# Kernel tuning notes

Measured on AMD Instinct MI355X. Metric: run time of the kernel, lower is better.

## Reference

```python
import jax, jax.numpy as jnp
import numpy as np
from jax import lax

B, C, H, W = 4, 256, 64, 64
O = 256
EPS = 1e-5


def setup_inputs() -> dict:
    key = jax.random.key(0)
    ks = jax.random.split(key, 20)
    s = 0.02
    d = {
        'input1': jax.random.normal(ks[0], (B, C, H, W), jnp.float32),
        'input2': jax.random.normal(ks[1], (B, C, H, W), jnp.float32),
        'wq1': jax.random.normal(ks[2], (C // 8, C), jnp.float32) * s,
        'bq1': jnp.zeros((C // 8,), jnp.float32),
        'wk1': jax.random.normal(ks[3], (C // 4, C), jnp.float32) * s,
        'bk1': jnp.zeros((C // 4,), jnp.float32),
        'wv1': jax.random.normal(ks[4], (C, C), jnp.float32) * s,
        'bv1': jnp.zeros((C,), jnp.float32),
        'wq2': jax.random.normal(ks[5], (C // 8, C), jnp.float32) * s,
        'bq2': jnp.zeros((C // 8,), jnp.float32),
        'wk2': jax.random.normal(ks[6], (C // 4, C), jnp.float32) * s,
        'bk2': jnp.zeros((C // 4,), jnp.float32),
        'wv2': jax.random.normal(ks[7], (C, C), jnp.float32) * s,
        'bv2': jnp.zeros((C,), jnp.float32),
        'gamma': jnp.asarray([0.1], jnp.float32),
        'w_cat': jax.random.normal(ks[8], (O, 2 * C, 3, 3), jnp.float32) * s,
        'bn_scale': jnp.ones((O,), jnp.float32),
        'bn_bias': jnp.zeros((O,), jnp.float32),
        'bn_mean': jnp.zeros((O,), jnp.float32),
        'bn_var': jnp.ones((O,), jnp.float32),
    }
    return d


def _conv1x1(x, w, b):
    # x: [B,C,H,W], w: [Co,C] -> [B,Co,H,W]
    return jnp.einsum('bchw,oc->bohw', x, w) + b[None, :, None, None]


def reference(input1, input2, wq1, bq1, wk1, bk1, wv1, bv1,
              wq2, bq2, wk2, bk2, wv2, bv2, gamma, w_cat,
              bn_scale, bn_bias, bn_mean, bn_var):
    b, c, h, w = input1.shape
    hw = h * w
    q1 = _conv1x1(input1, wq1, bq1)
    k1 = _conv1x1(input1, wk1, bk1).reshape(b, -1, hw)
    v1 = _conv1x1(input1, wv1, bv1).reshape(b, -1, hw)
    q2 = _conv1x1(input2, wq2, bq2)
    k2 = _conv1x1(input2, wk2, bk2).reshape(b, -1, hw)
    v2 = _conv1x1(input2, wv2, bv2).reshape(b, -1, hw)
    # concat q heads along channel -> [B, C/4, HW] -> [B, HW, C/4]
    q = jnp.concatenate([q1, q2], axis=1).reshape(b, -1, hw).transpose(0, 2, 1)
    # branch 1: [B,HW,HW] scores (no scaling, as in source)
    attn1 = jax.nn.softmax(jnp.einsum('bnc,bcm->bnm', q, k1), axis=-1)
    out1 = jnp.einsum('bcm,bnm->bcn', v1, attn1).reshape(b, c, h, w)
    out1 = gamma[0] * out1 + input1
    # branch 2
    attn2 = jax.nn.softmax(jnp.einsum('bnc,bcm->bnm', q, k2), axis=-1)
    out2 = jnp.einsum('bcm,bnm->bcn', v2, attn2).reshape(b, c, h, w)
    out2 = gamma[0] * out2 + input2
    # conv_cat: 3x3 conv (no bias) + BatchNorm (eval stats) + ReLU
    cat = jnp.concatenate([out1, out2], axis=1)
    conv = lax.conv_general_dilated(cat, w_cat, (1, 1), 'SAME',
                                    dimension_numbers=('NCHW', 'OIHW', 'NCHW'))
    inv = bn_scale / jnp.sqrt(bn_var + EPS)
    bn = conv * inv[None, :, None, None] + (bn_bias - bn_mean * inv)[None, :, None, None]
    feat_sum = jax.nn.relu(bn)
    return (feat_sum, out1, out2)
```

## Files before the change

### kernel.cpp

```cpp
#include <hip/hip_runtime.h>
#include <hip/hip_bf16.h>

#define HW 4096

#define KT_OFF   1048576
#define WTP_OFF  1572864
#define O1_OFF   4194304
#define WVB_OFF  1179648
#define XBF_OFF  1310720
#define WS_NEED  19398656ull
#define WS_NEED2 20463616ull

typedef short v8s  __attribute__((ext_vector_type(8)));
typedef float v16f __attribute__((ext_vector_type(16)));

#define LSTR 72
#define ZSTR 264
#define CPAD 20
#define PL_ROWS 128
#define PL_SZ  (2 * PL_ROWS * LSTR)
#define XP_SZ  (2 * 256 * LSTR)
#define XLHALF (4 * 66 * CPAD)
#define CPYCH  69696
#define CPYB   2230272
#define V5SL   4224

__device__ __forceinline__ unsigned short f2b(float f) {
    unsigned u = __float_as_uint(f);
    return (unsigned short)((u + 0x7fffu + ((u >> 16) & 1u)) >> 16);
}
__device__ __forceinline__ unsigned cvt_pk_bf16(float lo, float hi) {
    float2 f2; f2.x = lo; f2.y = hi;
    __hip_bfloat162 h = __float22bfloat162_rn(f2);
    unsigned r;
    __builtin_memcpy(&r, &h, 4);
    return r;
}
__device__ __forceinline__ v8s load8(const unsigned short* p) {
    union { uint2 u[2]; v8s v; } t;
    t.u[0] = *(const uint2*)p;
    t.u[1] = *(const uint2*)(p + 4);
    return t.v;
}

__global__ __launch_bounds__(256) void wprep_proj(
    const float* __restrict__ wq1, const float* __restrict__ wk1, const float* __restrict__ wv1,
    const float* __restrict__ wq2, const float* __restrict__ wk2, const float* __restrict__ wv2,
    float* __restrict__ wtp) {
    int idx = blockIdx.x * 256 + threadIdx.x;
    if (idx >= 2 * 256 * 352) return;
    int sel = idx / 90112;
    int r   = idx - sel * 90112;
    int c   = r / 352;
    int co  = r - c * 352;
    const float* w; int row;
    if (co < 32)      { w = sel ? wq2 : wq1; row = co; }
    else if (co < 96) { w = sel ? wk2 : wk1; row = co - 32; }
    else              { w = sel ? wv2 : wv1; row = co - 96; }
    wtp[idx] = w[row * 256 + c];
}

__global__ __launch_bounds__(256) void wprep_convw(const float* __restrict__ wcat,
                                                   unsigned short* __restrict__ wt) {
    int i = blockIdx.x * 256 + threadIdx.x;
    if (i >= 32 * 9 * 256 * 16) return;
    const int ci_l = i & 15;
    const int o    = (i >> 4) & 255;
    const int t2   = i >> 12;
    const int tap  = t2 % 9;
    const int chunk = t2 / 9;
    wt[i] = f2b(wcat[((size_t)o * 512 + chunk * 16 + ci_l) * 9 + tap]);
}

__global__ __launch_bounds__(256) void wprep_wv(const float* __restrict__ wv1,
                                                const float* __restrict__ wv2,
                                                unsigned short* __restrict__ out) {
    int i = blockIdx.x * 256 + threadIdx.x;
    if (i >= 131072) return;
    const float* src = (i < 65536) ? wv1 : wv2;
    out[i] = f2b(src[i & 65535]);
}

__global__ __launch_bounds__(256) void wprep_xbf(const float* __restrict__ x1,
                                                 const float* __restrict__ x2,
                                                 unsigned short* __restrict__ xbf) {
    const size_t e = ((size_t)blockIdx.x * 256 + threadIdx.x) * 8;
    if (e >= 8388608) return;
    const float* src = (e < 4194304) ? (x1 + e) : (x2 + (e - 4194304));
    const float4 a = *(const float4*)src;
    const float4 c = *(const float4*)(src + 4);
    uint4 o;
    o.x = cvt_pk_bf16(a.x, a.y); o.y = cvt_pk_bf16(a.z, a.w);
    o.z = cvt_pk_bf16(c.x, c.y); o.w = cvt_pk_bf16(c.z, c.w);
    *(uint4*)&xbf[e] = o;
}

__global__ __launch_bounds__(256) void proj_kernel(
    const float* __restrict__ x1, const float* __restrict__ x2,
    const float* __restrict__ bq1, const float* __restrict__ bk1,
    const float* __restrict__ bq2, const float* __restrict__ bk2,
    float* __restrict__ dout) {
    __shared__ __align__(16) float xls[256][64];
    const int tile = blockIdx.x, sel = blockIdx.y, b = blockIdx.z;
    const int n0 = tile * 64;
    const float* xb = (sel ? x2 : x1) + (size_t)b * 256 * HW;

    for (int i = threadIdx.x; i < 4096; i += 256) {
        const int row = i >> 4, c4 = (i & 15) * 4;
        *(float4*)&xls[row][c4] = *(const float4*)(xb + (size_t)row * HW + n0 + c4);
    }
    __syncthreads();

    const int n   = threadIdx.x & 63;
    const int cog = __builtin_amdgcn_readfirstlane(threadIdx.x >> 6);
    const float* bq = sel ? bq2 : bq1;
    const float* bk = sel ? bk2 : bk1;
    const float* wc = dout + WTP_OFF + (size_t)sel * 90112;
    unsigned short* qtg = (unsigned short*)dout + (size_t)b * HW * 64;
    unsigned short* ktg = (unsigned short*)dout + KT_OFF + (size_t)(sel * 4 + b) * HW * 64;

    for (int blk = 0; blk < 3; ++blk) {
        const int co0 = cog * 24 + blk * 8;
        float acc[8];
        const float* brow; int r0; bool isq;
        if (co0 < 32) { r0 = co0;      brow = bq; isq = true;  }
        else          { r0 = co0 - 32; brow = bk; isq = false; }
        #pragma unroll
        for (int k = 0; k < 8; ++k) acc[k] = brow[r0 + k];
        #pragma unroll 4
        for (int c = 0; c < 256; ++c) {
            const float xv = xls[c][n];
            const float4 w0 = *(const float4*)(wc + (size_t)c * 352 + co0);
            const float4 w1 = *(const float4*)(wc + (size_t)c * 352 + co0 + 4);
            acc[0] += xv * w0.x; acc[1] += xv * w0.y; acc[2] += xv * w0.z; acc[3] += xv * w0.w;
            acc[4] += xv * w1.x; acc[5] += xv * w1.y; acc[6] += xv * w1.z; acc[7] += xv * w1.w;
        }
        unsigned pk2[4];
        #pragma unroll
        for (int k = 0; k < 4; ++k) pk2[k] = cvt_pk_bf16(acc[2 * k], acc[2 * k + 1]);
        unsigned short* dst = isq ? (qtg + (size_t)(n0 + n) * 64 + sel * 32 + r0)
                                  : (ktg + (size_t)(n0 + n) * 64 + r0);
        *(uint4*)dst = *(const uint4*)pk2;
    }
}

template <int USEBF>
__global__ __launch_bounds__(512, 2) void attn_kernel(
    const float* __restrict__ in1, const float* __restrict__ in2,
    const unsigned short* __restrict__ xbf,
    const unsigned short* __restrict__ wvbf,
    const float* __restrict__ bv1, const float* __restrict__ bv2,
    const float* __restrict__ gamma_p,
    float* __restrict__ dout) {
    __shared__ __align__(16) unsigned short smem[PL_SZ + XP_SZ];
    __shared__ float rsums[128][2];
    __shared__ float lfin[128];

    const int bid = blockIdx.x;
    const int g   = bid & 7;
    const int qt  = bid >> 3;
    const int br  = g >> 2, b = g & 3;
    const int t = threadIdx.x;
    const int w = t >> 6, lane = t & 63, h = lane >> 5, l32 = lane & 31;

    const unsigned short* qtg = (const unsigned short*)dout + (size_t)b * HW * 64;
    const unsigned short* ktg = (const unsigned short*)dout + KT_OFF + (size_t)(br * 4 + b) * HW * 64;
    const float* xg = (br ? in2 : in1) + (size_t)b * 256 * HW;
    float* zo = dout + O1_OFF + (size_t)br * 4194304 + (size_t)b * 256 * HW;

    const int msub = (w & 1) * 32;
    const int nsub = (w >> 1) * 32;
    const int cs   = w & 3;
    const int nh   = w >> 2;
    const int koff = h * 8;

    unsigned short* plds = smem;
    unsigned short* xp   = smem + PL_SZ;

    v8s aq[4];
    #pragma unroll
    for (int ks = 0; ks < 4; ++ks)
        aq[ks] = *(const v8s*)(qtg + (size_t)(qt * 128 + nsub + l32) * 64 + ks * 16 + koff);

    const unsigned short* kpt = ktg + (size_t)(msub + l32) * 64 + koff;
    v8s kf[4];
    #pragma unroll
    for (int ks = 0; ks < 4; ++ks)
        kf[ks] = *(const v8s*)(kpt + ks * 16);

    const int m4 = (t & 15) * 4, r0i = t >> 4;
    const float* xgp = xg + (size_t)r0i * HW + m4;
    const unsigned short* xbp = xbf + (size_t)br * 4194304
                              + (size_t)b * 256 * HW + (size_t)r0i * HW + m4;

    uint2 xpk[8];
    if constexpr (USEBF) {
        #pragma unroll
        for (int j = 0; j < 8; ++j) xpk[j] = *(const uint2*)(xbp + (size_t)j * 32 * HW);
    } else {
        float4 xr0[8];
        #pragma unroll
        for (int j = 0; j < 8; ++j) xr0[j] = *(const float4*)(xgp + (size_t)j * 32 * HW);
        #pragma unroll
        for (int j = 0; j < 8; ++j) {
            xpk[j].x = cvt_pk_bf16(xr0[j].x, xr0[j].y);
            xpk[j].y = cvt_pk_bf16(xr0[j].z, xr0[j].w);
        }
    }

    v16f a00, a01, a10, a11;
    #pragma unroll
    for (int i = 0; i < 16; ++i) { a00[i] = 0.f; a01[i] = 0.f; a10[i] = 0.f; a11[i] = 0.f; }
    float racc = 0.f;

    #pragma unroll 1
    for (int mt = 0; mt < 64; ++mt) {
        const int cur = mt & 1;
        v16f s;
        #pragma unroll
        for (int i = 0; i < 16; ++i) s[i] = 0.f;
        #pragma unroll
        for (int ks = 0; ks < 4; ++ks)
            s = __builtin_amdgcn_mfma_f32_32x32x16_bf16(kf[ks], aq[ks], s, 0, 0, 0);
        const int mg = (mt < 63) ? (mt + 1) * 64 : 0;
        #pragma unroll
        for (int ks = 0; ks < 4; ++ks)
            kf[ks] = *(const v8s*)(kpt + (size_t)mg * 64 + ks * 16);
        float4 xr[8];
        if constexpr (!USEBF) {
            #pragma unroll
            for (int j = 0; j < 8; ++j)
                xr[j] = *(const float4*)(xgp + (size_t)j * 32 * HW + mg);
        }
        unsigned short* prow = plds + (size_t)(cur * PL_ROWS + nsub + l32) * LSTR + msub;
        #pragma unroll
        for (int rp = 0; rp < 8; ++rp) {
            const float e0 = __expf(s[2 * rp]);
            const float e1 = __expf(s[2 * rp + 1]);
            racc += e0 + e1;
            const int m0 = ((2 * rp) & 3) + 8 * (rp >> 1) + 4 * h;
            *(unsigned*)&prow[m0] = cvt_pk_bf16(e0, e1);
        }
        {
            unsigned short* xw = xp + (size_t)(cur * 256 + r0i) * LSTR + m4;
            #pragma unroll
            for (int j = 0; j < 8; ++j)
                *(uint2*)(xw + (size_t)j * 32 * LSTR) = xpk[j];
        }
        if constexpr (USEBF) {
            #pragma unroll
            for (int j = 0; j < 8; ++j)
                xpk[j] = *(const uint2*)(xbp + (size_t)j * 32 * HW + mg);
        }
        __syncthreads();
        {
            const unsigned short* xb0 = xp + (size_t)(cur * 256 + cs * 64 + l32) * LSTR;
            const unsigned short* xb1 = xb0 + (size_t)32 * LSTR;
            const unsigned short* pb0 = plds + (size_t)(cur * PL_ROWS + nh * 64 + l32) * LSTR;
            const unsigned short* pb1 = pb0 + (size_t)32 * LSTR;
            #pragma unroll
            for (int ks = 0; ks < 4; ++ks) {
                const int mo = ks * 16 + koff;
                const v8s xa0 = *(const v8s*)(xb0 + mo);
                const v8s xa1 = *(const v8s*)(xb1 + mo);
                const v8s pf0 = *(const v8s*)(pb0 + mo);
                const v8s pf1 = *(const v8s*)(pb1 + mo);
                a00 = __builtin_amdgcn_mfma_f32_32x32x16_bf16(xa0, pf0, a00, 0, 0, 0);
                a01 = __builtin_amdgcn_mfma_f32_32x32x16_bf16(xa0, pf1, a01, 0, 0, 0);
                a10 = __builtin_amdgcn_mfma_f32_32x32x16_bf16(xa1, pf0, a10, 0, 0, 0);
                a11 = __builtin_amdgcn_mfma_f32_32x32x16_bf16(xa1, pf1, a11, 0, 0, 0);
            }
        }
        if constexpr (!USEBF) {
            #pragma unroll
            for (int j = 0; j < 8; ++j) {
                xpk[j].x = cvt_pk_bf16(xr[j].x, xr[j].y);
                xpk[j].y = cvt_pk_bf16(xr[j].z, xr[j].w);
            }
        }
    }
    __syncthreads();
    {
        const float rtot = racc + __shfl_xor(racc, 32);
        if (lane < 32) rsums[nsub + l32][w & 1] = rtot;
    }
    __syncthreads();
    if (t < 128) lfin[t] = 1.0f / (rsums[t][0] + rsums[t][1]);
    __syncthreads();
    const float dn0 = lfin[nh * 64 + l32];
    const float dn1 = lfin[nh * 64 + 32 + l32];
    unsigned short (*zt)[ZSTR] = (unsigned short (*)[ZSTR])smem;
    #pragma unroll
    for (int rp = 0; rp < 8; ++rp) {
        const int r = rp * 2;
        const int c = cs * 64 + (r & 3) + 8 * (r >> 2) + 4 * h;
        const int n0r = nh * 64 + l32, n1r = nh * 64 + 32 + l32;
        *(unsigned*)&zt[n0r][c]      = cvt_pk_bf16(a00[r] * dn0, a00[r + 1] * dn0);
        *(unsigned*)&zt[n1r][c]      = cvt_pk_bf16(a01[r] * dn1, a01[r + 1] * dn1);
        *(unsigned*)&zt[n0r][c + 32] = cvt_pk_bf16(a10[r] * dn0, a10[r + 1] * dn0);
        *(unsigned*)&zt[n1r][c + 32] = cvt_pk_bf16(a11[r] * dn1, a11[r + 1] * dn1);
    }
    __syncthreads();
    const unsigned short* wvb = wvbf + (size_t)br * 65536;
    const float* bvp = br ? bv2 : bv1;
    const float gamma = gamma_p[0];
    const int ob = cs * 64;
    const int ncol = qt * 128 + nh * 64;
    v16f m00, m01, m10, m11;
    #pragma unroll
    for (int i = 0; i < 16; ++i) { m00[i] = 0.f; m01[i] = 0.f; m10[i] = 0.f; m11[i] = 0.f; }
    #pragma unroll
    for (int ks = 0; ks < 16; ++ks) {
        const int k = ks * 16 + koff;
        const v8s aA = *(const v8s*)(wvb + (size_t)(ob + l32) * 256 + k);
        const v8s aB = *(const v8s*)(wvb + (size_t)(ob + 32 + l32) * 256 + k);
        const v8s b0v = *(const v8s*)&zt[nh * 64 + l32][k];
        const v8s b1v = *(const v8s*)&zt[nh * 64 + 32 + l32][k];
        m00 = __builtin_amdgcn_mfma_f32_32x32x16_bf16(aA, b0v, m00, 0, 0, 0);
        m01 = __builtin_amdgcn_mfma_f32_32x32x16_bf16(aA, b1v, m01, 0, 0, 0);
        m10 = __builtin_amdgcn_mfma_f32_32x32x16_bf16(aB, b0v, m10, 0, 0, 0);
        m11 = __builtin_amdgcn_mfma_f32_32x32x16_bf16(aB, b1v, m11, 0, 0, 0);
    }
    #pragma unroll
    for (int r = 0; r < 16; ++r) {
        const int o = ob + (r & 3) + 8 * (r >> 2) + 4 * h;
        const float bvA = bvp[o], bvB = bvp[o + 32];
        const size_t base0 = (size_t)o * HW + ncol;
        const size_t base1 = (size_t)(o + 32) * HW + ncol;
        zo[base0 + l32]      = gamma * (m00[r] + bvA) + xg[base0 + l32];
        zo[base0 + 32 + l32] = gamma * (m01[r] + bvA) + xg[base0 + 32 + l32];
        zo[base1 + l32]      = gamma * (m10[r] + bvB) + xg[base1 + l32];
        zo[base1 + 32 + l32] = gamma * (m11[r] + bvB) + xg[base1 + 32 + l32];
    }
}

__global__ __launch_bounds__(256) void cpy_pad(const float* __restrict__ dsrc,
                                               unsigned short* __restrict__ cpy) {
    __shared__ float xls[16][65];
    const int hp = blockIdx.x, chunk = blockIdx.y, b = blockIdx.z;
    const int t = threadIdx.x;
    unsigned short* crow = cpy + (((size_t)(b * 32 + chunk) * 66 + hp) * 66) * 16;
    if (hp == 0 || hp == 65) {
        if (t < 132) *(uint4*)(crow + t * 8) = make_uint4(0, 0, 0, 0);
        return;
    }
    const int hh = hp - 1;
    const float* src = dsrc + O1_OFF + (size_t)(chunk < 16 ? 0 : 1) * 4194304
                     + (size_t)b * 1048576 + (size_t)((chunk & 15) * 16) * HW + (size_t)hh * 64;
    {
        const int ci = t >> 6, ww = t & 63;
        #pragma unroll
        for (int j = 0; j < 4; ++j)
            xls[ci + 4 * j][ww] = src[(size_t)(ci + 4 * j) * HW + ww];
    }
    __syncthreads();
    {
        const int wwp = t >> 2, q = t & 3;
        uint2 pk;
        pk.x = cvt_pk_bf16(xls[q * 4 + 0][wwp], xls[q * 4 + 1][wwp]);
        pk.y = cvt_pk_bf16(xls[q * 4 + 2][wwp], xls[q * 4 + 3][wwp]);
        *(uint2*)(crow + (size_t)(wwp + 1) * 16 + q * 4) = pk;
    }
    if (t < 4) {
        unsigned short* p = crow + (size_t)(t >> 1) * 65 * 16 + (t & 1) * 8;
        *(uint4*)p = make_uint4(0, 0, 0, 0);
    }
}

__global__ __launch_bounds__(256, 4) void conv_v5(
    const unsigned short* __restrict__ wt,
    const unsigned short* __restrict__ cpy,
    const float* __restrict__ bn_scale, const float* __restrict__ bn_bias,
    const float* __restrict__ bn_mean,  const float* __restrict__ bn_var,
    float* __restrict__ dout) {
    __shared__ __align__(16) unsigned short xl[2][V5SL];

    const int bid = blockIdx.x;
    const int lin = (bid & 7) * 128 + (bid >> 3);
    const int ot  = lin & 7;
    const int g   = lin >> 3;
    const int pt  = g & 31, b = g >> 5;
    const int h0  = pt * 2;
    const int t   = threadIdx.x;
    const int w   = t >> 6, lane = t & 63, h = lane >> 5, l32 = lane & 31;
    const int px  = w * 32 + l32;
    const int r0  = px >> 6, c0 = px & 63;

    const unsigned short* cb = cpy + (size_t)b * CPYB + (size_t)h0 * 66 * 16;
    const unsigned short* wb = wt + (size_t)(ot * 32 + l32) * 16 + h * 8;

    v16f acc;
    #pragma unroll
    for (int i = 0; i < 16; ++i) acc[i] = 0.f;

    uint4 xs[3]; bool xv[3];
    #pragma unroll
    for (int j = 0; j < 3; ++j) {
        const int idx = j * 256 + t;
        xv[j] = idx < 528;
        if (xv[j]) xs[j] = *(const uint4*)(cb + (size_t)idx * 8);
    }

    #pragma unroll 1
    for (int chunk = 0; chunk < 32; ++chunk) {
        const int cur = chunk & 1;
        #pragma unroll
        for (int j = 0; j < 3; ++j)
            if (xv[j]) *(uint4*)&xl[cur][(size_t)(j * 256 + t) * 8] = xs[j];
        v8s wf[9];
        {
            const unsigned short* wc = wb + (size_t)chunk * 36864;
            #pragma unroll
            for (int tap = 0; tap < 9; ++tap)
                wf[tap] = *(const v8s*)(wc + (size_t)tap * 4096);
        }
        if (chunk < 31) {
            const unsigned short* cn = cb + (size_t)(chunk + 1) * CPYCH;
            #pragma unroll
            for (int j = 0; j < 3; ++j)
                if (xv[j]) xs[j] = *(const uint4*)(cn + (size_t)(j * 256 + t) * 8);
        }
        __syncthreads();
        #pragma unroll
        for (int dy = 0; dy < 3; ++dy) {
            #pragma unroll
            for (int dx = 0; dx < 3; ++dx) {
                const v8s bf = *(const v8s*)&xl[cur][(size_t)((r0 + dy) * 66 + c0 + dx) * 16 + h * 8];
                acc = __builtin_amdgcn_mfma_f32_32x32x16_bf16(wf[dy * 3 + dx], bf, acc, 0, 0, 0);
            }
        }
    }
    const size_t gp = (size_t)(h0 + r0) * 64 + c0;
    #pragma unroll
    for (int r = 0; r < 16; ++r) {
        const int o_g = ot * 32 + (r & 3) + 8 * (r >> 2) + 4 * h;
        const float iv = bn_scale[o_g] * __frsqrt_rn(bn_var[o_g] + 1e-5f);
        const float ad = bn_bias[o_g] - bn_mean[o_g] * iv;
        float v = acc[r] * iv + ad;
        v = v > 0.f ? v : 0.f;
        dout[((size_t)b * 256 + o_g) * HW + gp] = v;
    }
}

__global__ __launch_bounds__(256) void conv_kernel(
    const unsigned short* __restrict__ wt,
    const float* __restrict__ bn_scale, const float* __restrict__ bn_bias,
    const float* __restrict__ bn_mean,  const float* __restrict__ bn_var,
    float* __restrict__ dout) {
    __shared__ __align__(16) unsigned short xl[2][4][66][CPAD];
    __shared__ __align__(16) unsigned short wl[2][9][64][CPAD];

    const int bid = blockIdx.x;
    const int xcd = bid & 7, j = bid >> 3;
    const int G   = xcd * 16 + (j >> 2);
    const int ot  = j & 3;
    const int pt  = G & 31;
    const int b   = G >> 5;
    const int h0 = pt * 2;
    const int t  = threadIdx.x;
    const int w  = t >> 6, lane = t & 63, h = lane >> 5, l32 = lane & 31;
    const int osub = (w & 1) * 32;
    const int ps0  = (w >> 1) * 64;

    int ldsoff[9], srcoff[9]; bool valid[9], inb[9];
    #pragma unroll
    for (int k = 0; k < 9; ++k) {
        const int i = t + k * 256;
        valid[k] = i < 2112;
        const int col = i % 66, rem = i / 66;
        const int row = rem & 3, cp = rem >> 2;
        const int hh = h0 + row - 1, ww = col - 1;
        inb[k] = (hh >= 0 && hh < 64 && ww >= 0 && ww < 64);
        srcoff[k] = 2 * cp * HW + (inb[k] ? hh * 64 + ww : 0);
        ldsoff[k] = (row * 66 + col) * CPAD + 2 * cp;
    }
    unsigned short* xlf = &xl[0][0][0][0];

    float inv[16], add[16];
    #pragma unroll
    for (int r = 0; r < 16; ++r) {
        const int o_g = ot * 64 + osub + (r & 3) + 8 * (r >> 2) + 4 * h;
        const float iv = bn_scale[o_g] * __frsqrt_rn(bn_var[o_g] + 1e-5f);
        inv[r] = iv;
        add[r] = bn_bias[o_g] - bn_mean[o_g] * iv;
    }

    v16f acc0, acc1;
    #pragma unroll
    for (int i = 0; i < 16; ++i) { acc0[i] = 0.f; acc1[i] = 0.f; }

    const float* bsrc = dout + O1_OFF + (size_t)b * 1048576;
    const unsigned short* wbase = wt + (size_t)(ot * 64) * 16;

    float xv0[9], xv1[9];
    uint2 wr[9];
    {
        const float* src = bsrc;
        #pragma unroll
        for (int k = 0; k < 9; ++k) {
            xv0[k] = 0.f; xv1[k] = 0.f;
            if (valid[k] && inb[k]) {
                const float* p = src + srcoff[k];
                xv0[k] = p[0]; xv1[k] = p[HW];
            }
        }
        #pragma unroll
        for (int u9 = 0; u9 < 9; ++u9) {
            const int u = t + u9 * 256;
            const int tap = u >> 8, rem2 = u & 255;
            const int o = rem2 >> 2, q = rem2 & 3;
            wr[u9] = *(const uint2*)(wbase + ((size_t)tap * 256 + o) * 16 + q * 4);
        }
    }

    #pragma unroll 1
    for (int chunk = 0; chunk < 32; ++chunk) {
        const int cur = chunk & 1;
        #pragma unroll
        for (int k = 0; k < 9; ++k)
            if (valid[k])
                *(unsigned*)&xlf[cur * XLHALF + ldsoff[k]] = cvt_pk_bf16(xv0[k], xv1[k]);
        #pragma unroll
        for (int u9 = 0; u9 < 9; ++u9) {
            const int u = t + u9 * 256;
            const int tap = u >> 8, rem2 = u & 255;
            const int o = rem2 >> 2, q = rem2 & 3;
            *(uint2*)&wl[cur][tap][o][q * 4] = wr[u9];
        }
        if (chunk < 31) {
            const int cn = chunk + 1;
            const float* src = bsrc + (size_t)(cn < 16 ? 0 : 1) * 4194304
                             + (size_t)((cn & 15) * 16) * HW;
            #pragma unroll
            for (int k = 0; k < 9; ++k) {
                xv0[k] = 0.f; xv1[k] = 0.f;
                if (valid[k] && inb[k]) {
                    const float* p = src + srcoff[k];
                    xv0[k] = p[0]; xv1[k] = p[HW];
                }
            }
            const unsigned short* wsl = wbase + (size_t)cn * 36864;
            #pragma unroll
            for (int u9 = 0; u9 < 9; ++u9) {
                const int u = t + u9 * 256;
                const int tap = u >> 8, rem2 = u & 255;
                const int o = rem2 >> 2, q = rem2 & 3;
                wr[u9] = *(const uint2*)(wsl + ((size_t)tap * 256 + o) * 16 + q * 4);
            }
        }
        __syncthreads();
        #pragma unroll
        for (int dy = 0; dy < 3; ++dy) {
            #pragma unroll
            for (int dx = 0; dx < 3; ++dx) {
                const v8s af = load8(&wl[cur][dy * 3 + dx][osub + l32][h * 8]);
                const int n0 = ps0 + l32, n1 = ps0 + 32 + l32;
                const v8s b0 = load8(&xl[cur][(n0 >> 6) + dy][(n0 & 63) + dx][h * 8]);
                const v8s b1 = load8(&xl[cur][(n1 >> 6) + dy][(n1 & 63) + dx][h * 8]);
                acc0 = __builtin_amdgcn_mfma_f32_32x32x16_bf16(af, b0, acc0, 0, 0, 0);
                acc1 = __builtin_amdgcn_mfma_f32_32x32x16_bf16(af, b1, acc1, 0, 0, 0);
            }
        }
    }
    const int px0 = ps0 + l32, px1 = ps0 + 32 + l32;
    const size_t gpx0 = (size_t)(h0 + (px0 >> 6)) * 64 + (px0 & 63);
    const size_t gpx1 = (size_t)(h0 + (px1 >> 6)) * 64 + (px1 & 63);
    #pragma unroll
    for (int r = 0; r < 16; ++r) {
        const int o_g = ot * 64 + osub + (r & 3) + 8 * (r >> 2) + 4 * h;
        const size_t obase = ((size_t)b * 256 + o_g) * HW;
        float v0 = acc0[r] * inv[r] + add[r];
        float v1 = acc1[r] * inv[r] + add[r];
        v0 = v0 > 0.f ? v0 : 0.f;
        v1 = v1 > 0.f ? v1 : 0.f;
        dout[obase + gpx0] = v0;
        dout[obase + gpx1] = v1;
    }
}

extern "C" void kernel_launch(void* const* d_in, const int* in_sizes, int n_in,
                              void* d_out, int out_size, void* d_ws, size_t ws_size,
                              hipStream_t stream) {
    (void)in_sizes; (void)n_in; (void)out_size;
    const float* x1   = (const float*)d_in[0];
    const float* x2   = (const float*)d_in[1];
    const float* wq1  = (const float*)d_in[2];
    const float* bq1  = (const float*)d_in[3];
    const float* wk1  = (const float*)d_in[4];
    const float* bk1  = (const float*)d_in[5];
    const float* wv1  = (const float*)d_in[6];
    const float* bv1  = (const float*)d_in[7];
    const float* wq2  = (const float*)d_in[8];
    const float* bq2  = (const float*)d_in[9];
    const float* wk2  = (const float*)d_in[10];
    const float* bk2  = (const float*)d_in[11];
    const float* wv2  = (const float*)d_in[12];
    const float* bv2  = (const float*)d_in[13];
    const float* gma  = (const float*)d_in[14];
    const float* wcat = (const float*)d_in[15];
    const float* bns  = (const float*)d_in[16];
    const float* bnb  = (const float*)d_in[17];
    const float* bnm  = (const float*)d_in[18];
    const float* bnv  = (const float*)d_in[19];

    float* out = (float*)d_out;
    unsigned short* wtc = (unsigned short*)d_ws;
    unsigned short* wvb = wtc + WVB_OFF;
    unsigned short* xbf = wtc + XBF_OFF;
    const bool use_bf  = ws_size >= WS_NEED;
    const bool use_cvb = ws_size >= WS_NEED2;

    wprep_proj<<<704, 256, 0, stream>>>(wq1, wk1, wv1, wq2, wk2, wv2, out + WTP_OFF);
    wprep_convw<<<4608, 256, 0, stream>>>(wcat, wtc);
    wprep_wv<<<512, 256, 0, stream>>>(wv1, wv2, wvb);
    if (use_bf) wprep_xbf<<<4096, 256, 0, stream>>>(x1, x2, xbf);
    proj_kernel<<<dim3(64, 2, 4), 256, 0, stream>>>(x1, x2, bq1, bk1, bq2, bk2, out);
    if (use_bf)
        attn_kernel<1><<<256, 512, 0, stream>>>(x1, x2, xbf, wvb, bv1, bv2, gma, out);
    else
        attn_kernel<0><<<256, 512, 0, stream>>>(x1, x2, xbf, wvb, bv1, bv2, gma, out);
    if (use_cvb) {
        cpy_pad<<<dim3(66, 32, 4), 256, 0, stream>>>(out, xbf);
        conv_v5<<<1024, 256, 0, stream>>>(wtc, xbf, bns, bnb, bnm, bnv, out);
    } else {
        conv_kernel<<<512, 256, 0, stream>>>(wtc, bns, bnb, bnm, bnv, out);
    }
}
```

Before: 465.5 us.

## Stage conv weights in LDS and compute 64x128 output tiles per block

The 3x3 conv kernel is restructured so each block covers 64 output channels over 128 pixels, with each wave owning two 32x32 MFMA accumulators. Weights are now staged cooperatively into double-buffered LDS rather than each lane loading its fragments straight from global memory. The grid is halved to 512 blocks and the BN scale/shift values are precomputed before the main loop. The goal is more reuse of each weight and input fragment and less redundant global weight traffic, at the cost of more LDS use, more registers and fewer blocks in flight.

```diff
diff --git a/kernel.cpp b/kernel.cpp
--- a/kernel.cpp
+++ b/kernel.cpp
@@ -23,7 +23,6 @@
 #define XLHALF (4 * 66 * CPAD)
 #define CPYCH  69696
 #define CPYB   2230272
-#define V5SL   4224
 
 __device__ __forceinline__ unsigned short f2b(float f) {
     unsigned u = __float_as_uint(f);
@@ -367,78 +366,120 @@
     }
 }
 
-__global__ __launch_bounds__(256, 4) void conv_v5(
+__global__ __launch_bounds__(256) void conv_v6(
     const unsigned short* __restrict__ wt,
     const unsigned short* __restrict__ cpy,
     const float* __restrict__ bn_scale, const float* __restrict__ bn_bias,
     const float* __restrict__ bn_mean,  const float* __restrict__ bn_var,
     float* __restrict__ dout) {
-    __shared__ __align__(16) unsigned short xl[2][V5SL];
+    __shared__ __align__(16) unsigned short xl[2][4][66][CPAD];
+    __shared__ __align__(16) unsigned short wl[2][9][64][CPAD];
 
     const int bid = blockIdx.x;
-    const int lin = (bid & 7) * 128 + (bid >> 3);
-    const int ot  = lin & 7;
-    const int g   = lin >> 3;
-    const int pt  = g & 31, b = g >> 5;
-    const int h0  = pt * 2;
-    const int t   = threadIdx.x;
-    const int w   = t >> 6, lane = t & 63, h = lane >> 5, l32 = lane & 31;
-    const int px  = w * 32 + l32;
-    const int r0  = px >> 6, c0 = px & 63;
+    const int xcd = bid & 7, j = bid >> 3;
+    const int G   = xcd * 16 + (j >> 2);
+    const int ot  = j & 3;
+    const int pt  = G & 31;
+    const int b   = G >> 5;
+    const int h0 = pt * 2;
+    const int t  = threadIdx.x;
+    const int w  = t >> 6, lane = t & 63, h = lane >> 5, l32 = lane & 31;
+    const int osub = (w & 1) * 32;
+    const int ps0  = (w >> 1) * 64;
 
     const unsigned short* cb = cpy + (size_t)b * CPYB + (size_t)h0 * 66 * 16;
-    const unsigned short* wb = wt + (size_t)(ot * 32 + l32) * 16 + h * 8;
-
-    v16f acc;
-    #pragma unroll
-    for (int i = 0; i < 16; ++i) acc[i] = 0.f;
-
-    uint4 xs[3]; bool xv[3];
-    #pragma unroll
-    for (int j = 0; j < 3; ++j) {
-        const int idx = j * 256 + t;
-        xv[j] = idx < 528;
-        if (xv[j]) xs[j] = *(const uint4*)(cb + (size_t)idx * 8);
+    unsigned short* xlf = &xl[0][0][0][0];
+
+    float inv[16], add[16];
+    #pragma unroll
+    for (int r = 0; r < 16; ++r) {
+        const int o_g = ot * 64 + osub + (r & 3) + 8 * (r >> 2) + 4 * h;
+        const float iv = bn_scale[o_g] * __frsqrt_rn(bn_var[o_g] + 1e-5f);
+        inv[r] = iv;
+        add[r] = bn_bias[o_g] - bn_mean[o_g] * iv;
+    }
+
+    v16f acc0, acc1;
+    #pragma unroll
+    for (int i = 0; i < 16; ++i) { acc0[i] = 0.f; acc1[i] = 0.f; }
+
+    const unsigned short* wbase = wt + (size_t)(ot * 64) * 16;
+
+    uint2 xs[5]; bool xv[5];
+    uint2 wr[9];
+    #pragma unroll
+    for (int k = 0; k < 5; ++k) {
+        const int u = t + k * 256;
+        xv[k] = u < 1056;
+        if (xv[k]) xs[k] = *(const uint2*)(cb + (size_t)u * 4);
+    }
+    #pragma unroll
+    for (int u9 = 0; u9 < 9; ++u9) {
+        const int u = t + u9 * 256;
+        const int tap = u >> 8, rem2 = u & 255;
+        const int o = rem2 >> 2, q = rem2 & 3;
+        wr[u9] = *(const uint2*)(wbase + ((size_t)tap * 256 + o) * 16 + q * 4);
     }
 
     #pragma unroll 1
     for (int chunk = 0; chunk < 32; ++chunk) {
         const int cur = chunk & 1;
         #pragma unroll
-        for (int j = 0; j < 3; ++j)
-            if (xv[j]) *(uint4*)&xl[cur][(size_t)(j * 256 + t) * 8] = xs[j];
-        v8s wf[9];
-        {
-            const unsigned short* wc = wb + (size_t)chunk * 36864;
-            #pragma unroll
-            for (int tap = 0; tap < 9; ++tap)
-                wf[tap] = *(const v8s*)(wc + (size_t)tap * 4096);
+        for (int k = 0; k < 5; ++k) {
+            if (xv[k]) {
+                const int u = t + k * 256;
+                const int p = u >> 2, q = u & 3;
+                *(uint2*)&xlf[cur * XLHALF + p * CPAD + q * 4] = xs[k];
+            }
+        }
+        #pragma unroll
+        for (int u9 = 0; u9 < 9; ++u9) {
+            const int u = t + u9 * 256;
+            const int tap = u >> 8, rem2 = u & 255;
+            const int o = rem2 >> 2, q = rem2 & 3;
+            *(uint2*)&wl[cur][tap][o][q * 4] = wr[u9];
         }
         if (chunk < 31) {
             const unsigned short* cn = cb + (size_t)(chunk + 1) * CPYCH;
             #pragma unroll
-            for (int j = 0; j < 3; ++j)
-                if (xv[j]) xs[j] = *(const uint4*)(cn + (size_t)(j * 256 + t) * 8);
+            for (int k = 0; k < 5; ++k)
+                if (xv[k]) xs[k] = *(const uint2*)(cn + (size_t)(t + k * 256) * 4);
+            const unsigned short* wsl = wbase + (size_t)(chunk + 1) * 36864;
+            #pragma unroll
+            for (int u9 = 0; u9 < 9; ++u9) {
+                const int u = t + u9 * 256;
+                const int tap = u >> 8, rem2 = u & 255;
+                const int o = rem2 >> 2, q = rem2 & 3;
+                wr[u9] = *(const uint2*)(wsl + ((size_t)tap * 256 + o) * 16 + q * 4);
+            }
         }
         __syncthreads();
         #pragma unroll
         for (int dy = 0; dy < 3; ++dy) {
             #pragma unroll
             for (int dx = 0; dx < 3; ++dx) {
-                const v8s bf = *(const v8s*)&xl[cur][(size_t)((r0 + dy) * 66 + c0 + dx) * 16 + h * 8];
-                acc = __builtin_amdgcn_mfma_f32_32x32x16_bf16(wf[dy * 3 + dx], bf, acc, 0, 0, 0);
-            }
-        }
-    }
-    const size_t gp = (size_t)(h0 + r0) * 64 + c0;
+                const v8s af = load8(&wl[cur][dy * 3 + dx][osub + l32][h * 8]);
+                const int n0 = ps0 + l32, n1 = ps0 + 32 + l32;
+                const v8s b0 = load8(&xl[cur][(n0 >> 6) + dy][(n0 & 63) + dx][h * 8]);
+                const v8s b1 = load8(&xl[cur][(n1 >> 6) + dy][(n1 & 63) + dx][h * 8]);
+                acc0 = __builtin_amdgcn_mfma_f32_32x32x16_bf16(af, b0, acc0, 0, 0, 0);
+                acc1 = __builtin_amdgcn_mfma_f32_32x32x16_bf16(af, b1, acc1, 0, 0, 0);
+            }
+        }
+    }
+    const int px0 = ps0 + l32, px1 = ps0 + 32 + l32;
+    const size_t gpx0 = (size_t)(h0 + (px0 >> 6)) * 64 + (px0 & 63);
+    const size_t gpx1 = (size_t)(h0 + (px1 >> 6)) * 64 + (px1 & 63);
     #pragma unroll
     for (int r = 0; r < 16; ++r) {
-        const int o_g = ot * 32 + (r & 3) + 8 * (r >> 2) + 4 * h;
-        const float iv = bn_scale[o_g] * __frsqrt_rn(bn_var[o_g] + 1e-5f);
-        const float ad = bn_bias[o_g] - bn_mean[o_g] * iv;
-        float v = acc[r] * iv + ad;
-        v = v > 0.f ? v : 0.f;
-        dout[((size_t)b * 256 + o_g) * HW + gp] = v;
+        const int o_g = ot * 64 + osub + (r & 3) + 8 * (r >> 2) + 4 * h;
+        const size_t obase = ((size_t)b * 256 + o_g) * HW;
+        float v0 = acc0[r] * inv[r] + add[r];
+        float v1 = acc1[r] * inv[r] + add[r];
+        v0 = v0 > 0.f ? v0 : 0.f;
+        v1 = v1 > 0.f ? v1 : 0.f;
+        dout[obase + gpx0] = v0;
+        dout[obase + gpx1] = v1;
     }
 }
 
@@ -621,7 +662,7 @@
         attn_kernel<0><<<256, 512, 0, stream>>>(x1, x2, xbf, wvb, bv1, bv2, gma, out);
     if (use_cvb) {
         cpy_pad<<<dim3(66, 32, 4), 256, 0, stream>>>(out, xbf);
-        conv_v5<<<1024, 256, 0, stream>>>(wtc, xbf, bns, bnb, bnm, bnv, out);
+        conv_v6<<<512, 256, 0, stream>>>(wtc, xbf, bns, bnb, bnm, bnv, out);
     } else {
         conv_kernel<<<512, 256, 0, stream>>>(wtc, bns, bnb, bnm, bnv, out);
     }
```

New measurement: 400.2 us. 1.16x faster.
